# Kernel tuning notes

Hardware: AMD Instinct MI355X
Metric: run time of the kernel (lower is better)

## Reference

```python
import jax, jax.numpy as jnp
import numpy as np

NY, NU, NH = 8, 8, 256
T, NB = 2048, 64


def setup_inputs() -> dict:
    key = jax.random.key(0)
    ks = jax.random.split(key, 10)
    return {
        "_y0": jax.random.normal(ks[0], (NB, NY), dtype=jnp.float32),
        "_U": jax.random.normal(ks[1], (T, NB, NU), dtype=jnp.float32),
        "lmbd_cont_real": jax.random.uniform(ks[2], (NH // 2,), dtype=jnp.float32),
        "lmbd_cont_imag": jax.random.uniform(ks[3], (NH // 2,), dtype=jnp.float32),
        "B": jax.random.normal(ks[4], (NH, NU), dtype=jnp.float32) / np.sqrt(NU).astype(np.float32),
        "multiplier_on_B": jnp.zeros((NH,), dtype=jnp.float32),
        "W_y2x": jax.random.normal(ks[5], (NH, NY), dtype=jnp.float32) / np.sqrt(NY).astype(np.float32),
        "b_y2x": jax.random.normal(ks[6], (NH,), dtype=jnp.float32) * 0.01,
        "W_x2y": jax.random.normal(ks[7], (NY, NH), dtype=jnp.float32) / np.sqrt(NH).astype(np.float32),
        "b_x2y": jax.random.normal(ks[8], (NY,), dtype=jnp.float32) * 0.01,
    }


def reference(_y0, _U, lmbd_cont_real, lmbd_cont_imag, B, multiplier_on_B,
              W_y2x, b_y2x, W_x2y, b_x2y):
    H2 = lmbd_cont_real.shape[0]
    # input drive: (T, NB, NH)
    Bu = jnp.einsum('tbu,hu->tbh', _U, B) * jnp.exp(multiplier_on_B)
    # stable complex-conjugate-pair eigenvalues
    r = jnp.exp(-jnp.abs(lmbd_cont_real))
    theta = (jnp.pi / 2) * lmbd_cont_imag
    re = r * jnp.cos(theta)
    im = r * jnp.sin(theta)
    # initial state from y0
    x0 = _y0 @ W_y2x.T + b_y2x  # (NB, NH)

    def step(x, bu):
        x1, x2 = x[:, :H2], x[:, H2:]
        # A = [[diag(re), -diag(im)], [diag(im), diag(re)]]; x <- x A^T + bu
        nx = jnp.concatenate([re * x1 - im * x2, im * x1 + re * x2], axis=1) + bu
        return nx, nx

    _, X = jax.lax.scan(step, x0, Bu)  # X: (T, NB, NH)
    Y = X @ W_x2y.T + b_x2y  # (T, NB, NY)
    return Y
```

## Files before the change

kernel.cpp:

```cpp
#include <hip/hip_runtime.h>
#include <math.h>

#define T_   2048
#define NB_  64
#define NU_  8
#define NY_  8
#define NH_  256
#define H2_  128
#define CCH  64
#define LCH  32
#define TT_  4

static const float PI_HALF = 1.5707963267948966f;


__global__ __launch_bounds__(64) void k_local(
    const float* __restrict__ U, const float* __restrict__ lr,
    const float* __restrict__ li, const float* __restrict__ B,
    const float* __restrict__ mult, float* __restrict__ buf)
{
    const int k = blockIdx.x >> 6;
    const int b = blockIdx.x & 63;
    const int j = threadIdx.x;
    const int p1 = j, p2 = j + 64;

    float r1  = expf(-fabsf(lr[p1]));
    float t1  = PI_HALF * li[p1];
    float re1 = r1 * cosf(t1), im1 = r1 * sinf(t1);
    float r2  = expf(-fabsf(lr[p2]));
    float t2  = PI_HALF * li[p2];
    float re2 = r2 * cosf(t2), im2 = r2 * sinf(t2);

    float B1[NU_], B2[NU_], B3[NU_], B4[NU_];
    {
        float s1 = expf(mult[j]),      s2 = expf(mult[j+128]);
        float s3 = expf(mult[j+64]),   s4 = expf(mult[j+192]);
        #pragma unroll
        for (int i = 0; i < NU_; i++) {
            B1[i] = B[(j      )*NU_ + i] * s1;
            B2[i] = B[(j + 128)*NU_ + i] * s2;
            B3[i] = B[(j +  64)*NU_ + i] * s3;
            B4[i] = B[(j + 192)*NU_ + i] * s4;
        }
    }

    __shared__ float uS[LCH*NU_];
    {
        int t = j >> 1, half = j & 1;
        float4 v = *(const float4*)(U + ((size_t)(k*LCH + t)*NB_ + b)*NU_ + half*4);
        ((float4*)uS)[j] = v;
    }
    __syncthreads();

    float x1a=0.f, x2a=0.f, x1b=0.f, x2b=0.f;
    #pragma unroll 8
    for (int t = 0; t < LCH; t++) {
        float4 u0 = ((const float4*)uS)[2*t+0];
        float4 u1 = ((const float4*)uS)[2*t+1];
        float u[NU_] = {u0.x,u0.y,u0.z,u0.w,u1.x,u1.y,u1.z,u1.w};
        float bu1=0.f, bu2=0.f, bu3=0.f, bu4=0.f;
        #pragma unroll
        for (int i = 0; i < NU_; i++) {
            bu1 = fmaf(u[i], B1[i], bu1);
            bu2 = fmaf(u[i], B2[i], bu2);
            bu3 = fmaf(u[i], B3[i], bu3);
            bu4 = fmaf(u[i], B4[i], bu4);
        }
        float n1a = fmaf(re1, x1a, fmaf(-im1, x2a, bu1));
        float n2a = fmaf(im1, x1a, fmaf( re1, x2a, bu2));
        float n1b = fmaf(re2, x1b, fmaf(-im2, x2b, bu3));
        float n2b = fmaf(im2, x1b, fmaf( re2, x2b, bu4));
        x1a=n1a; x2a=n2a; x1b=n1b; x2b=n2b;
    }

    float* base = buf + ((size_t)(k*NB_ + b))*(H2_*2);
    *(float2*)(base + 2*j)       = make_float2(x1a, x2a);
    *(float2*)(base + 128 + 2*j) = make_float2(x1b, x2b);
}

__global__ __launch_bounds__(256) void k_prefix(
    const float* __restrict__ y0, const float* __restrict__ lr,
    const float* __restrict__ li, const float* __restrict__ Wy2x,
    const float* __restrict__ by2x, float* __restrict__ buf)
{
    const int g = blockIdx.x*256 + threadIdx.x;
    const int b = g >> 7;
    const int h = g & 127;

    float x1 = by2x[h], x2 = by2x[h+H2_];
    #pragma unroll
    for (int y = 0; y < NY_; y++) {
        float yy = y0[b*NY_ + y];
        x1 = fmaf(yy, Wy2x[h*NY_ + y],        x1);
        x2 = fmaf(yy, Wy2x[(h+H2_)*NY_ + y],  x2);
    }

    float rL  = expf(-(float)LCH * fabsf(lr[h]));
    float thL = (float)LCH * PI_HALF * li[h];
    float reL = rL * cosf(thL), imL = rL * sinf(thL);

    #pragma unroll 8
    for (int k = 0; k < CCH; k++) {
        float* p = buf + ((size_t)(k*NB_ + b))*(H2_*2) + 2*h;
        float2 c = *(const float2*)p;
        *(float2*)p = make_float2(x1, x2);
        float n1 = fmaf(reL, x1, fmaf(-imL, x2, c.x));
        float n2 = fmaf(imL, x1, fmaf( reL, x2, c.y));
        x1 = n1; x2 = n2;
    }
}

__global__ __launch_bounds__(64) void k_emit(
    const float* __restrict__ U, const float* __restrict__ lr,
    const float* __restrict__ li, const float* __restrict__ B,
    const float* __restrict__ mult, const float* __restrict__ Wx2y,
    const float* __restrict__ bx2y, const float* __restrict__ buf,
    float* __restrict__ Y)
{
    const int k = blockIdx.x >> 6;
    const int b = blockIdx.x & 63;
    const int j = threadIdx.x;
    const int p1 = j, p2 = j + 64;

    float r1  = expf(-fabsf(lr[p1]));
    float t1  = PI_HALF * li[p1];
    float re1 = r1 * cosf(t1), im1 = r1 * sinf(t1);
    float r2  = expf(-fabsf(lr[p2]));
    float t2  = PI_HALF * li[p2];
    float re2 = r2 * cosf(t2), im2 = r2 * sinf(t2);

    float B1[NU_], B2[NU_], B3[NU_], B4[NU_];
    {
        float s1 = expf(mult[j]),      s2 = expf(mult[j+128]);
        float s3 = expf(mult[j+64]),   s4 = expf(mult[j+192]);
        #pragma unroll
        for (int i = 0; i < NU_; i++) {
            B1[i] = B[(j      )*NU_ + i] * s1;
            B2[i] = B[(j + 128)*NU_ + i] * s2;
            B3[i] = B[(j +  64)*NU_ + i] * s3;
            B4[i] = B[(j + 192)*NU_ + i] * s4;
        }
    }

    float W1[NY_], W2[NY_], W3[NY_], W4[NY_];
    #pragma unroll
    for (int y = 0; y < NY_; y++) {
        W1[y] = Wx2y[y*NH_ + j      ];
        W2[y] = Wx2y[y*NH_ + j + 128];
        W3[y] = Wx2y[y*NH_ + j +  64];
        W4[y] = Wx2y[y*NH_ + j + 192];
    }
    const float biasv = bx2y[j & 7];

    __shared__ float uS[LCH*NU_];
    __shared__ float pS[64*36];
    {
        int t = j >> 1, half = j & 1;
        float4 v = *(const float4*)(U + ((size_t)(k*LCH + t)*NB_ + b)*NU_ + half*4);
        ((float4*)uS)[j] = v;
    }

    const float* base = buf + ((size_t)(k*NB_ + b))*(H2_*2);
    float2 i1 = *(const float2*)(base + 2*j);
    float2 i2 = *(const float2*)(base + 128 + 2*j);
    float x1a=i1.x, x2a=i1.y, x1b=i2.x, x2b=i2.y;
    __syncthreads();

    float* outk = Y + ((size_t)k*LCH*NB_ + b)*NY_;

    for (int tt = 0; tt < LCH/TT_; tt++) {
        float p[TT_*NY_];
        #pragma unroll
        for (int t4 = 0; t4 < TT_; t4++) {
            int t = tt*TT_ + t4;
            float4 u0 = ((const float4*)uS)[2*t+0];
            float4 u1 = ((const float4*)uS)[2*t+1];
            float u[NU_] = {u0.x,u0.y,u0.z,u0.w,u1.x,u1.y,u1.z,u1.w};
            float bu1=0.f, bu2=0.f, bu3=0.f, bu4=0.f;
            #pragma unroll
            for (int i = 0; i < NU_; i++) {
                bu1 = fmaf(u[i], B1[i], bu1);
                bu2 = fmaf(u[i], B2[i], bu2);
                bu3 = fmaf(u[i], B3[i], bu3);
                bu4 = fmaf(u[i], B4[i], bu4);
            }
            float n1a = fmaf(re1, x1a, fmaf(-im1, x2a, bu1));
            float n2a = fmaf(im1, x1a, fmaf( re1, x2a, bu2));
            float n1b = fmaf(re2, x1b, fmaf(-im2, x2b, bu3));
            float n2b = fmaf(im2, x1b, fmaf( re2, x2b, bu4));
            x1a=n1a; x2a=n2a; x1b=n1b; x2b=n2b;

            #pragma unroll
            for (int y = 0; y < NY_; y++) {
                p[t4*NY_ + y] = fmaf(x1a, W1[y], fmaf(x2a, W2[y],
                                fmaf(x1b, W3[y], x2b * W4[y])));
            }
        }
        float* row = pS + j*36;
        #pragma unroll
        for (int g = 0; g < 8; g++) {
            *(float4*)(row + 4*g) =
                make_float4(p[4*g+0], p[4*g+1], p[4*g+2], p[4*g+3]);
        }
        __syncthreads();
        {
            const int idx = j & 31;
            const int lh  = j >> 5;
            float s0=0.f, s1=0.f, s2=0.f, s3=0.f;
            #pragma unroll
            for (int s = 0; s < 32; s += 4) {
                s0 += pS[(lh*32 + s+0)*36 + idx];
                s1 += pS[(lh*32 + s+1)*36 + idx];
                s2 += pS[(lh*32 + s+2)*36 + idx];
                s3 += pS[(lh*32 + s+3)*36 + idx];
            }
            float sum = (s0+s1) + (s2+s3);
            sum += __shfl_xor(sum, 32, 64);
            if (j < 32) {
                int t4 = j >> 3, y = j & 7;
                outk[(size_t)(tt*TT_ + t4)*NB_*NY_ + y] = sum + biasv;
            }
        }
        __syncthreads();
    }
}

extern "C" void kernel_launch(void* const* d_in, const int* in_sizes, int n_in,
                              void* d_out, int out_size, void* d_ws, size_t ws_size,
                              hipStream_t stream) {
    const float* y0   = (const float*)d_in[0];
    const float* U    = (const float*)d_in[1];
    const float* lr   = (const float*)d_in[2];
    const float* li   = (const float*)d_in[3];
    const float* B    = (const float*)d_in[4];
    const float* mult = (const float*)d_in[5];
    const float* Wy2x = (const float*)d_in[6];
    const float* by2x = (const float*)d_in[7];
    const float* Wx2y = (const float*)d_in[8];
    const float* bx2y = (const float*)d_in[9];
    float* Y = (float*)d_out;

    float* buf = (float*)d_ws;

    k_local <<<CCH*NB_, 64,  0, stream>>>(U, lr, li, B, mult, buf);
    k_prefix<<<(NB_*H2_)/256, 256, 0, stream>>>(y0, lr, li, Wy2x, by2x, buf);
    k_emit  <<<CCH*NB_, 64,  0, stream>>>(U, lr, li, B, mult, Wx2y, bx2y, buf, Y);
}
```

Baseline: 112.1 us.

## Use more, shorter scan chunks and separate prefix input/output buffers

Halves the chunk length (LCH 32->16) and doubles the chunk count, so k_local and k_emit launch twice as many blocks with shorter serial recurrences. k_prefix now runs on 64-thread blocks to spread across more CUs, and it writes to a separate init buffer instead of updating in place. The emit reduction is resized for two timesteps per group and adds an extra shuffle. The serial prefix loop becomes twice as long, and the two buffers double workspace traffic.

```diff
diff --git a/kernel.cpp b/kernel.cpp
--- a/kernel.cpp
+++ b/kernel.cpp
@@ -7,28 +7,28 @@
 #define NY_  8
 #define NH_  256
 #define H2_  128
-#define CCH  64
-#define LCH  32
-#define TT_  4
-
+#define CCH  128
+#define LCH  16
+#define TT_  2
+
+#define BUF_FLOATS (CCH*NB_*H2_*2)
 static const float PI_HALF = 1.5707963267948966f;
 
 
-__global__ __launch_bounds__(64) void k_local(
+__global__ __launch_bounds__(64, 8) void k_local(
     const float* __restrict__ U, const float* __restrict__ lr,
     const float* __restrict__ li, const float* __restrict__ B,
-    const float* __restrict__ mult, float* __restrict__ buf)
+    const float* __restrict__ mult, float* __restrict__ c_buf)
 {
     const int k = blockIdx.x >> 6;
     const int b = blockIdx.x & 63;
     const int j = threadIdx.x;
-    const int p1 = j, p2 = j + 64;
-
-    float r1  = expf(-fabsf(lr[p1]));
-    float t1  = PI_HALF * li[p1];
+
+    float r1  = expf(-fabsf(lr[j]));
+    float t1  = PI_HALF * li[j];
     float re1 = r1 * cosf(t1), im1 = r1 * sinf(t1);
-    float r2  = expf(-fabsf(lr[p2]));
-    float t2  = PI_HALF * li[p2];
+    float r2  = expf(-fabsf(lr[j+64]));
+    float t2  = PI_HALF * li[j+64];
     float re2 = r2 * cosf(t2), im2 = r2 * sinf(t2);
 
     float B1[NU_], B2[NU_], B3[NU_], B4[NU_];
@@ -45,7 +45,7 @@
     }
 
     __shared__ float uS[LCH*NU_];
-    {
+    if (j < 32) {
         int t = j >> 1, half = j & 1;
         float4 v = *(const float4*)(U + ((size_t)(k*LCH + t)*NB_ + b)*NU_ + half*4);
         ((float4*)uS)[j] = v;
@@ -53,7 +53,7 @@
     __syncthreads();
 
     float x1a=0.f, x2a=0.f, x1b=0.f, x2b=0.f;
-    #pragma unroll 8
+    #pragma unroll
     for (int t = 0; t < LCH; t++) {
         float4 u0 = ((const float4*)uS)[2*t+0];
         float4 u1 = ((const float4*)uS)[2*t+1];
@@ -73,17 +73,18 @@
         x1a=n1a; x2a=n2a; x1b=n1b; x2b=n2b;
     }
 
-    float* base = buf + ((size_t)(k*NB_ + b))*(H2_*2);
+    float* base = c_buf + ((size_t)(k*NB_ + b))*(H2_*2);
     *(float2*)(base + 2*j)       = make_float2(x1a, x2a);
     *(float2*)(base + 128 + 2*j) = make_float2(x1b, x2b);
 }
 
-__global__ __launch_bounds__(256) void k_prefix(
+__global__ __launch_bounds__(64) void k_prefix(
     const float* __restrict__ y0, const float* __restrict__ lr,
     const float* __restrict__ li, const float* __restrict__ Wy2x,
-    const float* __restrict__ by2x, float* __restrict__ buf)
+    const float* __restrict__ by2x, const float* __restrict__ c_buf,
+    float* __restrict__ init_buf)
 {
-    const int g = blockIdx.x*256 + threadIdx.x;
+    const int g = blockIdx.x*64 + threadIdx.x;
     const int b = g >> 7;
     const int h = g & 127;
 
@@ -99,34 +100,35 @@
     float thL = (float)LCH * PI_HALF * li[h];
     float reL = rL * cosf(thL), imL = rL * sinf(thL);
 
+    const size_t stride = NB_*(size_t)(H2_*2);
+    const size_t off    = (size_t)b*(H2_*2) + 2*h;
+
     #pragma unroll 8
     for (int k = 0; k < CCH; k++) {
-        float* p = buf + ((size_t)(k*NB_ + b))*(H2_*2) + 2*h;
-        float2 c = *(const float2*)p;
-        *(float2*)p = make_float2(x1, x2);
+        float2 c = *(const float2*)(c_buf + k*stride + off);
+        *(float2*)(init_buf + k*stride + off) = make_float2(x1, x2);
         float n1 = fmaf(reL, x1, fmaf(-imL, x2, c.x));
         float n2 = fmaf(imL, x1, fmaf( reL, x2, c.y));
         x1 = n1; x2 = n2;
     }
 }
 
-__global__ __launch_bounds__(64) void k_emit(
+__global__ __launch_bounds__(64, 8) void k_emit(
     const float* __restrict__ U, const float* __restrict__ lr,
     const float* __restrict__ li, const float* __restrict__ B,
     const float* __restrict__ mult, const float* __restrict__ Wx2y,
-    const float* __restrict__ bx2y, const float* __restrict__ buf,
+    const float* __restrict__ bx2y, const float* __restrict__ init_buf,
     float* __restrict__ Y)
 {
     const int k = blockIdx.x >> 6;
     const int b = blockIdx.x & 63;
     const int j = threadIdx.x;
-    const int p1 = j, p2 = j + 64;
-
-    float r1  = expf(-fabsf(lr[p1]));
-    float t1  = PI_HALF * li[p1];
+
+    float r1  = expf(-fabsf(lr[j]));
+    float t1  = PI_HALF * li[j];
     float re1 = r1 * cosf(t1), im1 = r1 * sinf(t1);
-    float r2  = expf(-fabsf(lr[p2]));
-    float t2  = PI_HALF * li[p2];
+    float r2  = expf(-fabsf(lr[j+64]));
+    float t2  = PI_HALF * li[j+64];
     float re2 = r2 * cosf(t2), im2 = r2 * sinf(t2);
 
     float B1[NU_], B2[NU_], B3[NU_], B4[NU_];
@@ -153,14 +155,14 @@
     const float biasv = bx2y[j & 7];
 
     __shared__ float uS[LCH*NU_];
-    __shared__ float pS[64*36];
-    {
+    __shared__ float pS[64*17];
+    if (j < 32) {
         int t = j >> 1, half = j & 1;
         float4 v = *(const float4*)(U + ((size_t)(k*LCH + t)*NB_ + b)*NU_ + half*4);
         ((float4*)uS)[j] = v;
     }
 
-    const float* base = buf + ((size_t)(k*NB_ + b))*(H2_*2);
+    const float* base = init_buf + ((size_t)(k*NB_ + b))*(H2_*2);
     float2 i1 = *(const float2*)(base + 2*j);
     float2 i2 = *(const float2*)(base + 128 + 2*j);
     float x1a=i1.x, x2a=i1.y, x1b=i2.x, x2b=i2.y;
@@ -168,6 +170,7 @@
 
     float* outk = Y + ((size_t)k*LCH*NB_ + b)*NY_;
 
+    #pragma unroll
     for (int tt = 0; tt < LCH/TT_; tt++) {
         float p[TT_*NY_];
         #pragma unroll
@@ -196,27 +199,25 @@
                                 fmaf(x1b, W3[y], x2b * W4[y])));
             }
         }
-        float* row = pS + j*36;
-        #pragma unroll
-        for (int g = 0; g < 8; g++) {
-            *(float4*)(row + 4*g) =
-                make_float4(p[4*g+0], p[4*g+1], p[4*g+2], p[4*g+3]);
-        }
+        float* row = pS + j*17;
+        #pragma unroll
+        for (int i = 0; i < TT_*NY_; i++) row[i] = p[i];
         __syncthreads();
         {
-            const int idx = j & 31;
-            const int lh  = j >> 5;
+            const int c = j & 15;
+            const int g = j >> 4;
             float s0=0.f, s1=0.f, s2=0.f, s3=0.f;
             #pragma unroll
-            for (int s = 0; s < 32; s += 4) {
-                s0 += pS[(lh*32 + s+0)*36 + idx];
-                s1 += pS[(lh*32 + s+1)*36 + idx];
-                s2 += pS[(lh*32 + s+2)*36 + idx];
-                s3 += pS[(lh*32 + s+3)*36 + idx];
+            for (int s = 0; s < 16; s += 4) {
+                s0 += pS[(g*16 + s+0)*17 + c];
+                s1 += pS[(g*16 + s+1)*17 + c];
+                s2 += pS[(g*16 + s+2)*17 + c];
+                s3 += pS[(g*16 + s+3)*17 + c];
             }
             float sum = (s0+s1) + (s2+s3);
+            sum += __shfl_xor(sum, 16, 64);
             sum += __shfl_xor(sum, 32, 64);
-            if (j < 32) {
+            if (j < 16) {
                 int t4 = j >> 3, y = j & 7;
                 outk[(size_t)(tt*TT_ + t4)*NB_*NY_ + y] = sum + biasv;
             }
@@ -240,9 +241,10 @@
     const float* bx2y = (const float*)d_in[9];
     float* Y = (float*)d_out;
 
-    float* buf = (float*)d_ws;
-
-    k_local <<<CCH*NB_, 64,  0, stream>>>(U, lr, li, B, mult, buf);
-    k_prefix<<<(NB_*H2_)/256, 256, 0, stream>>>(y0, lr, li, Wy2x, by2x, buf);
-    k_emit  <<<CCH*NB_, 64,  0, stream>>>(U, lr, li, B, mult, Wx2y, bx2y, buf, Y);
-}
+    float* c_buf    = (float*)d_ws;
+    float* init_buf = c_buf + BUF_FLOATS;
+
+    k_local <<<CCH*NB_, 64, 0, stream>>>(U, lr, li, B, mult, c_buf);
+    k_prefix<<<(NB_*H2_)/64, 64, 0, stream>>>(y0, lr, li, Wy2x, by2x, c_buf, init_buf);
+    k_emit  <<<CCH*NB_, 64, 0, stream>>>(U, lr, li, B, mult, Wx2y, bx2y, init_buf, Y);
+}
```

After: 331.0 us. 195% more time.
